# Performance work log

Hardware: AMD Instinct MI355X
Metric: run time of the kernel (lower is better)

## Reference

```python
import jax, jax.numpy as jnp
import numpy as np

N = 50000      # nodes
E = 800000     # edges
F_IN = 256
H1, D1 = 4, 32   # conv1 heads, per-head dim (hidden_features)
H2, D2 = 1, 32   # conv2 heads, per-head dim (out_features)
NEG_SLOPE = 0.2


def setup_inputs():
    key = jax.random.key(0)
    ks = jax.random.split(key, 12)
    x = jax.random.normal(ks[0], (N, F_IN), dtype=jnp.float32)
    src = jax.random.randint(ks[1], (E,), 0, N, dtype=jnp.int32)
    dst = jax.random.randint(ks[2], (E,), 0, N, dtype=jnp.int32)
    s = 0.05
    W1 = jax.random.normal(ks[3], (F_IN, H1 * D1), dtype=jnp.float32) * s
    al1 = jax.random.normal(ks[4], (H1, D1), dtype=jnp.float32) * s
    ar1 = jax.random.normal(ks[5], (H1, D1), dtype=jnp.float32) * s
    b1 = jnp.zeros((H1 * D1,), dtype=jnp.float32)
    W2 = jax.random.normal(ks[6], (H1 * D1, H2 * D2), dtype=jnp.float32) * s
    al2 = jax.random.normal(ks[7], (H2, D2), dtype=jnp.float32) * s
    ar2 = jax.random.normal(ks[8], (H2, D2), dtype=jnp.float32) * s
    b2 = jnp.zeros((H2 * D2,), dtype=jnp.float32)
    return {"x": x, "W1": W1, "al1": al1, "ar1": ar1, "b1": b1,
            "W2": W2, "al2": al2, "ar2": ar2, "b2": b2,
            "src": src, "dst": dst}


def gat_layer(x, W, al, ar, b, src, dst, H, D):
    # x: [N, F] -> feat: [N, H, D]
    feat = (x @ W).reshape(-1, H, D)
    el = jnp.sum(feat * al, axis=-1)   # [N, H]
    er = jnp.sum(feat * ar, axis=-1)   # [N, H]
    # per-edge attention logits, LeakyReLU
    e = jax.nn.leaky_relu(el[src] + er[dst], negative_slope=NEG_SLOPE)  # [E, H]
    # edge softmax over destination neighborhoods (stable)
    m = jax.ops.segment_max(e, dst, num_segments=N)          # [N, H]
    m = jnp.where(jnp.isfinite(m), m, 0.0)                   # guard zero-in-degree
    ee = jnp.exp(e - m[dst])                                 # [E, H]
    z = jax.ops.segment_sum(ee, dst, num_segments=N)         # [N, H]
    a = ee / jnp.maximum(z[dst], 1e-16)                      # [E, H]
    # weighted message aggregation
    msg = feat[src] * a[:, :, None]                          # [E, H, D]
    rst = jax.ops.segment_sum(msg, dst, num_segments=N)      # [N, H, D]
    return (rst + b.reshape(1, H, D)).reshape(-1, H * D)     # flatten(1)


def reference(x, W1, al1, ar1, b1, W2, al2, ar2, b2, src, dst):
    # dropouts are identity in eval mode; is_out_layer=True => no activation
    h = gat_layer(x, W1, al1, ar1, b1, src, dst, H1, D1)     # [N, H1*D1]
    out = gat_layer(h, W2, al2, ar2, b2, src, dst, H2, D2)   # [N, H2*D2]
    return out
```

## Files before the change

### kernel.cpp

```cpp
#include <hip/hip_runtime.h>

constexpr int F_IN = 256;
constexpr int H1 = 4, D1 = 32, F1 = H1 * D1;
constexpr int H2 = 1, D2 = 32, F2 = H2 * D2;
constexpr float NEG = 0.2f;

constexpr int BW = 128;
constexpr int NBUK_MAX = 512;
constexpr int CB = 128;

typedef short short8 __attribute__((ext_vector_type(8)));
typedef float f32x4 __attribute__((ext_vector_type(4)));

__device__ inline float bf2f(unsigned short u) {
    unsigned int x = ((unsigned int)u) << 16;
    return __builtin_bit_cast(float, x);
}
__device__ inline unsigned short f2bf(float f) {
    __bf16 h = (__bf16)f;
    return __builtin_bit_cast(unsigned short, h);
}

__global__ __launch_bounds__(256) void chist(const int* __restrict__ dst,
                                             unsigned int* __restrict__ HcT,
                                             int E, int nbuk) {
    __shared__ unsigned int h[NBUK_MAX];
    int tid = threadIdx.x;
    for (int i = tid; i < nbuk; i += 256) h[i] = 0;
    __syncthreads();
    int epb = (E + CB - 1) / CB;
    int e0 = blockIdx.x * epb, e1 = min(e0 + epb, E);
    for (int e = e0 + tid; e < e1; e += 256)
        atomicAdd(&h[dst[e] >> 7], 1u);
    __syncthreads();
    for (int i = tid; i < nbuk; i += 256) HcT[(size_t)i * CB + blockIdx.x] = h[i];
}

__global__ __launch_bounds__(512) void bscan(const unsigned int* __restrict__ HcT,
                                             unsigned int* __restrict__ Bb,
                                             unsigned int* __restrict__ S, int nbuk) {
    __shared__ unsigned int tot[NBUK_MAX];
    int t = threadIdx.x;
    unsigned int run = 0;
    if (t < nbuk) {
        const uint4* row = (const uint4*)(HcT + (size_t)t * CB);
#pragma unroll 8
        for (int b4 = 0; b4 < CB / 4; ++b4) {
            uint4 v = row[b4];
            int b = b4 * 4;
            Bb[(size_t)(b + 0) * nbuk + t] = run; run += v.x;
            Bb[(size_t)(b + 1) * nbuk + t] = run; run += v.y;
            Bb[(size_t)(b + 2) * nbuk + t] = run; run += v.z;
            Bb[(size_t)(b + 3) * nbuk + t] = run; run += v.w;
        }
    }
    tot[t] = (t < nbuk) ? run : 0;
    __syncthreads();
    for (int o = 1; o < NBUK_MAX; o <<= 1) {
        unsigned int v = (t >= o) ? tot[t - o] : 0;
        __syncthreads();
        tot[t] += v;
        __syncthreads();
    }
    if (t < nbuk) S[t] = tot[t] - run;
    if (t == nbuk - 1) S[nbuk] = tot[t];
}

__global__ __launch_bounds__(256) void cscat(const int* __restrict__ src,
                                             const int* __restrict__ dst,
                                             const unsigned int* __restrict__ Bb,
                                             const unsigned int* __restrict__ S,
                                             unsigned int* __restrict__ pairs, int E, int nbuk) {
    __shared__ unsigned int h[NBUK_MAX];
    int tid = threadIdx.x;
    for (int i = tid; i < nbuk; i += 256) h[i] = 0;
    __syncthreads();
    int epb = (E + CB - 1) / CB;
    int e0 = blockIdx.x * epb, e1 = min(e0 + epb, E);
    const unsigned int* bb = Bb + (size_t)blockIdx.x * nbuk;
    for (int e = e0 + tid; e < e1; e += 256) {
        int d = dst[e];
        int k = d >> 7;
        unsigned int r = atomicAdd(&h[k], 1u);
        unsigned int p = S[k] + bb[k] + r;
        pairs[p] = ((unsigned int)(d & 127) << 17) | (unsigned int)src[e];
    }
}

__global__ __launch_bounds__(256) void fscat(const unsigned int* __restrict__ pairs,
                                             const unsigned int* __restrict__ S,
                                             int* __restrict__ off, int* __restrict__ csr,
                                             int n, int E) {
    int k = blockIdx.x;
    int tid = threadIdx.x;
    unsigned int s0 = S[k], s1 = S[k + 1];
    __shared__ unsigned int cnt[BW];
    __shared__ unsigned int ex[BW];
    if (tid < BW) cnt[tid] = 0;
    __syncthreads();
    for (unsigned int i = s0 + tid; i < s1; i += 256)
        atomicAdd(&cnt[pairs[i] >> 17], 1u);
    __syncthreads();
    unsigned int orig = (tid < BW) ? cnt[tid] : 0;
    if (tid < BW) ex[tid] = orig;
    __syncthreads();
    for (int o = 1; o < BW; o <<= 1) {
        unsigned int v = (tid < BW && tid >= (unsigned)o) ? ex[tid - o] : 0;
        __syncthreads();
        if (tid < BW) ex[tid] += v;
        __syncthreads();
    }
    if (tid < BW) {
        ex[tid] -= orig;
        int node = k * BW + tid;
        if (node < n) off[node] = (int)(s0 + ex[tid]);
    }
    if (tid < BW) cnt[tid] = 0;
    __syncthreads();
    for (unsigned int i = s0 + tid; i < s1; i += 256) {
        unsigned int pr = pairs[i];
        int loc = pr >> 17;
        unsigned int r = atomicAdd(&cnt[loc], 1u);
        csr[s0 + ex[loc] + r] = (int)(pr & 0x1FFFFu);
    }
    if (k == 0 && tid == 0) off[n] = E;
}

__device__ inline void wsplit_one(const float* W, unsigned short* Wh, unsigned short* Wl,
                                  int idx, int C) {
    int j    = idx & 7;
    int lane = (idx >> 3) & 63;
    int t    = idx >> 9;
    int FC   = C >> 4;
    int fc   = t % FC, ks = t / FC;
    int k = ks * 32 + (lane >> 4) * 8 + j;
    int c = fc * 16 + (lane & 15);
    float v = W[(size_t)k * C + c];
    __bf16 h = (__bf16)v;
    float hv = (float)h;
    __bf16 lo = (__bf16)(v - hv);
    Wh[idx] = __builtin_bit_cast(unsigned short, h);
    Wl[idx] = __builtin_bit_cast(unsigned short, lo);
}
__global__ void wsplit_swz2(const float* __restrict__ W1, unsigned short* __restrict__ W1h,
                            unsigned short* __restrict__ W1l,
                            const float* __restrict__ W2, unsigned short* __restrict__ W2h,
                            unsigned short* __restrict__ W2l) {
    int idx = blockIdx.x * 256 + threadIdx.x;
    constexpr int N1 = F_IN * F1;
    if (idx < N1) wsplit_one(W1, W1h, W1l, idx, F1);
    else if (idx < N1 + F1 * F2) wsplit_one(W2, W2h, W2l, idx - N1, F2);
}

constexpr int BM1 = 32;
__global__ __launch_bounds__(256) void gemm1_mfma(
    const float* __restrict__ X,
    const unsigned short* __restrict__ Wh,
    const unsigned short* __restrict__ Wl,
    const float* __restrict__ alv, const float* __restrict__ arv,
    unsigned short* __restrict__ outb,
    float* __restrict__ el, float* __restrict__ er, int n)
{
    __shared__ float xs[64 * BM1 * 4];
    const int tid  = threadIdx.x;
    const int lane = tid & 63;
    const int wid  = tid >> 6;
    const int wrow = (wid >> 1) * 16;
    const int wcol = (wid & 1) * 64;
    const int wc16 = wcol >> 4;
    const int row0 = blockIdx.x * BM1;
    const int l16  = lane & 15;
    const int khi  = lane >> 4;

    {
        int r = lane & 31;
        int sub = lane >> 5;
        int gr = row0 + r;
        gr = gr < n ? gr : (n - 1);
        const float* rowp = X + (size_t)gr * F_IN;
#pragma unroll
        for (int i = 0; i < 8; ++i) {
            int kc = wid * 16 + i * 2;
            const float* srcp = rowp + (kc + sub) * 4;
            float* dstf = &xs[kc * BM1 * 4];
            __builtin_amdgcn_global_load_lds(
                (const __attribute__((address_space(1))) unsigned int*)srcp,
                (__attribute__((address_space(3))) unsigned int*)dstf,
                16, 0, 0);
        }
    }
    asm volatile("s_waitcnt vmcnt(0)" ::: "memory");
    __syncthreads();

    f32x4 acc[4];
#pragma unroll
    for (int ni = 0; ni < 4; ++ni) acc[ni] = f32x4{0.f, 0.f, 0.f, 0.f};

    const int rt = wrow + l16;

#pragma unroll
    for (int ks = 0; ks < 8; ++ks) {
        const int kc = ks * 8 + khi * 2;

        short8 bh[4], bl[4];
#pragma unroll
        for (int ni = 0; ni < 4; ++ni) {
            int base = ((ks * 8 + wc16 + ni) * 64 + lane) * 8;
            bh[ni] = *(const short8*)(Wh + base);
            bl[ni] = *(const short8*)(Wl + base);
        }

        float4 xa0 = *(const float4*)&xs[(kc + 0) * BM1 * 4 + rt * 4];
        float4 xa1 = *(const float4*)&xs[(kc + 1) * BM1 * 4 + rt * 4];
        float v[8] = {xa0.x, xa0.y, xa0.z, xa0.w, xa1.x, xa1.y, xa1.z, xa1.w};
        short8 ah, al8;
#pragma unroll
        for (int j = 0; j < 8; ++j) {
            __bf16 h = (__bf16)v[j];
            float hv = (float)h;
            __bf16 lo = (__bf16)(v[j] - hv);
            ah[j] = __builtin_bit_cast(short, h);
            al8[j] = __builtin_bit_cast(short, lo);
        }

#pragma unroll
        for (int ni = 0; ni < 4; ++ni) {
            acc[ni] = __builtin_amdgcn_mfma_f32_16x16x32_bf16(al8, bh[ni], acc[ni], 0, 0, 0);
            acc[ni] = __builtin_amdgcn_mfma_f32_16x16x32_bf16(ah, bl[ni], acc[ni], 0, 0, 0);
            acc[ni] = __builtin_amdgcn_mfma_f32_16x16x32_bf16(ah, bh[ni], acc[ni], 0, 0, 0);
        }
    }

    const int hh0 = wcol >> 5;
    float alr[2][2], arr[2][2];
#pragma unroll
    for (int t = 0; t < 2; ++t) {
        int head = hh0 + t;
        alr[t][0] = alv[head * 32 + l16];
        alr[t][1] = alv[head * 32 + 16 + l16];
        arr[t][0] = arv[head * 32 + l16];
        arr[t][1] = arv[head * 32 + 16 + l16];
    }

    int rbase = row0 + wrow + khi * 4;
#pragma unroll
    for (int rr = 0; rr < 4; ++rr) {
        int row = rbase + rr;
        bool ok = row < n;
        if (ok) {
#pragma unroll
            for (int ni = 0; ni < 4; ++ni)
                outb[(size_t)row * F1 + wcol + ni * 16 + l16] = f2bf(acc[ni][rr]);
        }
#pragma unroll
        for (int t = 0; t < 2; ++t) {
            float pel = acc[2 * t][rr] * alr[t][0] + acc[2 * t + 1][rr] * alr[t][1];
            float per = acc[2 * t][rr] * arr[t][0] + acc[2 * t + 1][rr] * arr[t][1];
#pragma unroll
            for (int o = 1; o < 16; o <<= 1) {
                pel += __shfl_xor(pel, o);
                per += __shfl_xor(per, o);
            }
            if (ok && l16 == 0) {
                el[(size_t)row * H1 + hh0 + t] = pel;
                er[(size_t)row * H1 + hh0 + t] = per;
            }
        }
    }
}

constexpr int BM2 = 64;
__global__ __launch_bounds__(256) void gemm2_mfma(
    const float* __restrict__ X,
    const unsigned short* __restrict__ Wh,
    const unsigned short* __restrict__ Wl,
    const float* __restrict__ alv, const float* __restrict__ arv,
    float* __restrict__ out,
    float* __restrict__ el, float* __restrict__ er, int n)
{
    __shared__ float xs[32 * BM2 * 4];
    const int tid  = threadIdx.x;
    const int lane = tid & 63;
    const int wid  = tid >> 6;
    const int wrow = wid * 16;
    const int row0 = blockIdx.x * BM2;
    const int l16  = lane & 15;
    const int khi  = lane >> 4;

    {
        int gr = row0 + lane;
        gr = gr < n ? gr : (n - 1);
        const float* rowp = X + (size_t)gr * F1;
#pragma unroll
        for (int i = 0; i < 8; ++i) {
            int kc = wid * 8 + i;
            const float* srcp = rowp + kc * 4;
            float* dstf = &xs[kc * BM2 * 4];
            __builtin_amdgcn_global_load_lds(
                (const __attribute__((address_space(1))) unsigned int*)srcp,
                (__attribute__((address_space(3))) unsigned int*)dstf,
                16, 0, 0);
        }
    }
    asm volatile("s_waitcnt vmcnt(0)" ::: "memory");
    __syncthreads();

    f32x4 acc[2];
#pragma unroll
    for (int ni = 0; ni < 2; ++ni) acc[ni] = f32x4{0.f, 0.f, 0.f, 0.f};

    const int rt = wrow + l16;

#pragma unroll
    for (int ks = 0; ks < 4; ++ks) {
        const int kc = ks * 8 + khi * 2;

        short8 bh[2], bl[2];
#pragma unroll
        for (int ni = 0; ni < 2; ++ni) {
            int base = ((ks * 2 + ni) * 64 + lane) * 8;
            bh[ni] = *(const short8*)(Wh + base);
            bl[ni] = *(const short8*)(Wl + base);
        }

        float4 xa0 = *(const float4*)&xs[(kc + 0) * BM2 * 4 + rt * 4];
        float4 xa1 = *(const float4*)&xs[(kc + 1) * BM2 * 4 + rt * 4];
        float v[8] = {xa0.x, xa0.y, xa0.z, xa0.w, xa1.x, xa1.y, xa1.z, xa1.w};
        short8 ah, al8;
#pragma unroll
        for (int j = 0; j < 8; ++j) {
            __bf16 h = (__bf16)v[j];
            float hv = (float)h;
            __bf16 lo = (__bf16)(v[j] - hv);
            ah[j] = __builtin_bit_cast(short, h);
            al8[j] = __builtin_bit_cast(short, lo);
        }

#pragma unroll
        for (int ni = 0; ni < 2; ++ni) {
            acc[ni] = __builtin_amdgcn_mfma_f32_16x16x32_bf16(al8, bh[ni], acc[ni], 0, 0, 0);
            acc[ni] = __builtin_amdgcn_mfma_f32_16x16x32_bf16(ah, bl[ni], acc[ni], 0, 0, 0);
            acc[ni] = __builtin_amdgcn_mfma_f32_16x16x32_bf16(ah, bh[ni], acc[ni], 0, 0, 0);
        }
    }

    float al0 = alv[l16], al1c = alv[16 + l16];
    float ar0 = arv[l16], ar1c = arv[16 + l16];

    int rbase = row0 + wrow + khi * 4;
#pragma unroll
    for (int rr = 0; rr < 4; ++rr) {
        int row = rbase + rr;
        bool ok = row < n;
        if (ok) {
#pragma unroll
            for (int ni = 0; ni < 2; ++ni)
                out[(size_t)row * F2 + ni * 16 + l16] = acc[ni][rr];
        }
        float pel = acc[0][rr] * al0 + acc[1][rr] * al1c;
        float per = acc[0][rr] * ar0 + acc[1][rr] * ar1c;
#pragma unroll
        for (int o = 1; o < 16; o <<= 1) {
            pel += __shfl_xor(pel, o);
            per += __shfl_xor(per, o);
        }
        if (ok && l16 == 0) {
            el[row] = pel;
            er[row] = per;
        }
    }
}

__global__ __launch_bounds__(256) void agg1_kernel(
    const int* __restrict__ off, const int* __restrict__ csr_src,
    const unsigned short* __restrict__ featb, const float* __restrict__ el,
    const float* __restrict__ er, const float* __restrict__ b,
    float* __restrict__ out, int n)
{
    int wid = (blockIdx.x * 256 + threadIdx.x) >> 6;
    int lane = threadIdx.x & 63;
    if (wid >= n) return;
    int c0 = (lane & 31) * 4;
    int h = (lane & 31) >> 3;
    int half = lane >> 5;
    float erv = er[(size_t)wid * H1 + h];
    float sw = 0.f;
    float4 acc = {0.f, 0.f, 0.f, 0.f};
    int jb = off[wid], je = off[wid + 1];
    int j = jb + half;
    for (; j + 6 < je; j += 8) {
        int s0 = csr_src[j];
        int s1 = csr_src[j + 2];
        int s2 = csr_src[j + 4];
        int s3 = csr_src[j + 6];
        ushort4 u0 = *(const ushort4*)(featb + (size_t)s0 * F1 + c0);
        ushort4 u1 = *(const ushort4*)(featb + (size_t)s1 * F1 + c0);
        ushort4 u2 = *(const ushort4*)(featb + (size_t)s2 * F1 + c0);
        ushort4 u3 = *(const ushort4*)(featb + (size_t)s3 * F1 + c0);
        float t0 = el[(size_t)s0 * H1 + h] + erv;
        float t1 = el[(size_t)s1 * H1 + h] + erv;
        float t2 = el[(size_t)s2 * H1 + h] + erv;
        float t3 = el[(size_t)s3 * H1 + h] + erv;
        t0 = t0 > 0.f ? t0 : NEG * t0;
        t1 = t1 > 0.f ? t1 : NEG * t1;
        t2 = t2 > 0.f ? t2 : NEG * t2;
        t3 = t3 > 0.f ? t3 : NEG * t3;
        float w0 = __expf(t0), w1 = __expf(t1), w2 = __expf(t2), w3 = __expf(t3);
        sw += (w0 + w1) + (w2 + w3);
        acc.x = fmaf(w0, bf2f(u0.x), fmaf(w1, bf2f(u1.x), fmaf(w2, bf2f(u2.x), fmaf(w3, bf2f(u3.x), acc.x))));
        acc.y = fmaf(w0, bf2f(u0.y), fmaf(w1, bf2f(u1.y), fmaf(w2, bf2f(u2.y), fmaf(w3, bf2f(u3.y), acc.y))));
        acc.z = fmaf(w0, bf2f(u0.z), fmaf(w1, bf2f(u1.z), fmaf(w2, bf2f(u2.z), fmaf(w3, bf2f(u3.z), acc.z))));
        acc.w = fmaf(w0, bf2f(u0.w), fmaf(w1, bf2f(u1.w), fmaf(w2, bf2f(u2.w), fmaf(w3, bf2f(u3.w), acc.w))));
    }
    for (; j < je; j += 2) {
        int s = csr_src[j];
        ushort4 u = *(const ushort4*)(featb + (size_t)s * F1 + c0);
        float t = el[(size_t)s * H1 + h] + erv;
        t = t > 0.f ? t : NEG * t;
        float w = __expf(t);
        sw += w;
        acc.x = fmaf(w, bf2f(u.x), acc.x);
        acc.y = fmaf(w, bf2f(u.y), acc.y);
        acc.z = fmaf(w, bf2f(u.z), acc.z);
        acc.w = fmaf(w, bf2f(u.w), acc.w);
    }
    acc.x += __shfl_xor(acc.x, 32);
    acc.y += __shfl_xor(acc.y, 32);
    acc.z += __shfl_xor(acc.z, 32);
    acc.w += __shfl_xor(acc.w, 32);
    sw    += __shfl_xor(sw, 32);
    if (half == 0) {
        float inv = 1.f / fmaxf(sw, 1e-16f);
        float4 bb = *(const float4*)(b + c0);
        float4 t = {acc.x * inv + bb.x, acc.y * inv + bb.y,
                    acc.z * inv + bb.z, acc.w * inv + bb.w};
        *(float4*)(out + (size_t)wid * F1 + c0) = t;
    }
}

__global__ __launch_bounds__(256) void agg2_kernel(
    const int* __restrict__ off, const int* __restrict__ csr_src,
    const float* __restrict__ feat, const float* __restrict__ el,
    const float* __restrict__ er, const float* __restrict__ b,
    float* __restrict__ out, int n)
{
    int wid = (blockIdx.x * 256 + threadIdx.x) >> 6;
    int lane = threadIdx.x & 63;
    if (wid >= n) return;
    int c0 = (lane & 7) * 4;
    int grp = lane >> 3;
    float erv = er[wid];
    float sw = 0.f;
    float4 acc = {0.f, 0.f, 0.f, 0.f};
    int jb = off[wid], je = off[wid + 1];
    int j = jb + grp;
    for (; j + 8 < je; j += 16) {
        int s0 = csr_src[j];
        int s1 = csr_src[j + 8];
        float4 f0 = *(const float4*)(feat + (size_t)s0 * F2 + c0);
        float4 f1 = *(const float4*)(feat + (size_t)s1 * F2 + c0);
        float t0 = el[s0] + erv;
        float t1 = el[s1] + erv;
        t0 = t0 > 0.f ? t0 : NEG * t0;
        t1 = t1 > 0.f ? t1 : NEG * t1;
        float w0 = __expf(t0);
        float w1 = __expf(t1);
        sw += w0 + w1;
        acc.x = fmaf(w0, f0.x, fmaf(w1, f1.x, acc.x));
        acc.y = fmaf(w0, f0.y, fmaf(w1, f1.y, acc.y));
        acc.z = fmaf(w0, f0.z, fmaf(w1, f1.z, acc.z));
        acc.w = fmaf(w0, f0.w, fmaf(w1, f1.w, acc.w));
    }
    for (; j < je; j += 8) {
        int s = csr_src[j];
        float4 f = *(const float4*)(feat + (size_t)s * F2 + c0);
        float t = el[s] + erv;
        t = t > 0.f ? t : NEG * t;
        float w = __expf(t);
        sw += w;
        acc.x = fmaf(w, f.x, acc.x);
        acc.y = fmaf(w, f.y, acc.y);
        acc.z = fmaf(w, f.z, acc.z);
        acc.w = fmaf(w, f.w, acc.w);
    }
#pragma unroll
    for (int o = 8; o < 64; o <<= 1) {
        acc.x += __shfl_xor(acc.x, o);
        acc.y += __shfl_xor(acc.y, o);
        acc.z += __shfl_xor(acc.z, o);
        acc.w += __shfl_xor(acc.w, o);
        sw    += __shfl_xor(sw, o);
    }
    if (lane < 8) {
        float inv = 1.f / fmaxf(sw, 1e-16f);
        float4 bb = *(const float4*)(b + c0);
        float4 t = {acc.x * inv + bb.x, acc.y * inv + bb.y,
                    acc.z * inv + bb.z, acc.w * inv + bb.w};
        *(float4*)(out + (size_t)wid * F2 + c0) = t;
    }
}

extern "C" void kernel_launch(void* const* d_in, const int* in_sizes, int n_in,
                              void* d_out, int out_size, void* d_ws, size_t ws_size,
                              hipStream_t stream) {
    const float* x   = (const float*)d_in[0];
    const float* W1  = (const float*)d_in[1];
    const float* al1 = (const float*)d_in[2];
    const float* ar1 = (const float*)d_in[3];
    const float* b1  = (const float*)d_in[4];
    const float* W2  = (const float*)d_in[5];
    const float* al2 = (const float*)d_in[6];
    const float* ar2 = (const float*)d_in[7];
    const float* b2  = (const float*)d_in[8];
    const int*   src = (const int*)d_in[9];
    const int*   dst = (const int*)d_in[10];

    const int N = in_sizes[0] / F_IN;
    const int E = in_sizes[9];
    const int NBUK = (N + BW - 1) / BW;

    char* w = (char*)d_ws;
    size_t o = 0;
    auto alloc = [&](size_t bytes) { size_t cur = o; o += (bytes + 255) & ~255ULL; return cur; };
    int*   off   = (int*)  (w + alloc((size_t)(N + 1) * 4));
    int*   csr   = (int*)  (w + alloc((size_t)E * 4));
    unsigned int* pairs = (unsigned int*)(w + alloc((size_t)E * 4));
    unsigned int* HcT = (unsigned int*)(w + alloc((size_t)CB * NBUK * 4));
    unsigned int* Bb  = (unsigned int*)(w + alloc((size_t)CB * NBUK * 4));
    unsigned int* S   = (unsigned int*)(w + alloc((size_t)(NBUK + 1) * 4));
    unsigned short* feat1b = (unsigned short*)(w + alloc((size_t)N * F1 * 2));
    float* el1   = (float*)(w + alloc((size_t)N * H1 * 4));
    float* er1   = (float*)(w + alloc((size_t)N * H1 * 4));
    float* h1    = (float*)(w + alloc((size_t)N * F1 * 4));
    float* feat2 = (float*)(w + alloc((size_t)N * F2 * 4));
    float* el2   = (float*)(w + alloc((size_t)N * H2 * 4));
    float* er2   = (float*)(w + alloc((size_t)N * H2 * 4));
    unsigned short* W1h = (unsigned short*)(w + alloc((size_t)F_IN * F1 * 2));
    unsigned short* W1l = (unsigned short*)(w + alloc((size_t)F_IN * F1 * 2));
    unsigned short* W2h = (unsigned short*)(w + alloc((size_t)F1 * F2 * 2));
    unsigned short* W2l = (unsigned short*)(w + alloc((size_t)F1 * F2 * 2));
    (void)ws_size; (void)n_in; (void)out_size;

    chist<<<CB, 256, 0, stream>>>(dst, HcT, E, NBUK);
    bscan<<<1, 512, 0, stream>>>(HcT, Bb, S, NBUK);
    cscat<<<CB, 256, 0, stream>>>(src, dst, Bb, S, pairs, E, NBUK);
    fscat<<<NBUK, 256, 0, stream>>>(pairs, S, off, csr, N, E);

    wsplit_swz2<<<(F_IN * F1 + F1 * F2 + 255) / 256, 256, 0, stream>>>(
        W1, W1h, W1l, W2, W2h, W2l);

    gemm1_mfma<<<(N + BM1 - 1) / BM1, 256, 0, stream>>>(
        x, W1h, W1l, al1, ar1, feat1b, el1, er1, N);
    agg1_kernel<<<(N + 3) / 4, 256, 0, stream>>>(off, csr, feat1b, el1, er1, b1, h1, N);

    gemm2_mfma<<<(N + BM2 - 1) / BM2, 256, 0, stream>>>(
        h1, W2h, W2l, al2, ar2, feat2, el2, er2, N);
    agg2_kernel<<<(N + 3) / 4, 256, 0, stream>>>(off, csr, feat2, el2, er2, b2, (float*)d_out, N);
}
```

Measured before the change: 149.7 us.

## Double gemm1 row tile and prefetch weight fragments one k-step ahead

Gemm1 now handles 64 rows per block, with each wave computing two 16-row MFMA tiles, so every loaded weight fragment (high and low bf16 halves) is reused across twice as many rows. The weight loads for the next k-step are double-buffered in registers so global loads overlap the current MFMAs. This halves the grid size and increases register and LDS use per block, which may reduce occupancy.

```diff
diff --git a/kernel.cpp b/kernel.cpp
--- a/kernel.cpp
+++ b/kernel.cpp
@@ -152,7 +152,7 @@
     else if (idx < N1 + F1 * F2) wsplit_one(W2, W2h, W2l, idx - N1, F2);
 }
 
-constexpr int BM1 = 32;
+constexpr int BM1 = 64;
 __global__ __launch_bounds__(256) void gemm1_mfma(
     const float* __restrict__ X,
     const unsigned short* __restrict__ Wh,
@@ -165,7 +165,7 @@
     const int tid  = threadIdx.x;
     const int lane = tid & 63;
     const int wid  = tid >> 6;
-    const int wrow = (wid >> 1) * 16;
+    const int wrow = (wid >> 1) * 32;
     const int wcol = (wid & 1) * 64;
     const int wc16 = wcol >> 4;
     const int row0 = blockIdx.x * BM1;
@@ -173,15 +173,13 @@
     const int khi  = lane >> 4;
 
     {
-        int r = lane & 31;
-        int sub = lane >> 5;
-        int gr = row0 + r;
+        int gr = row0 + lane;
         gr = gr < n ? gr : (n - 1);
         const float* rowp = X + (size_t)gr * F_IN;
 #pragma unroll
-        for (int i = 0; i < 8; ++i) {
-            int kc = wid * 16 + i * 2;
-            const float* srcp = rowp + (kc + sub) * 4;
+        for (int i = 0; i < 16; ++i) {
+            int kc = wid * 16 + i;
+            const float* srcp = rowp + kc * 4;
             float* dstf = &xs[kc * BM1 * 4];
             __builtin_amdgcn_global_load_lds(
                 (const __attribute__((address_space(1))) unsigned int*)srcp,
@@ -192,43 +190,58 @@
     asm volatile("s_waitcnt vmcnt(0)" ::: "memory");
     __syncthreads();
 
-    f32x4 acc[4];
-#pragma unroll
-    for (int ni = 0; ni < 4; ++ni) acc[ni] = f32x4{0.f, 0.f, 0.f, 0.f};
-
-    const int rt = wrow + l16;
+    f32x4 acc[2][4];
+#pragma unroll
+    for (int mi = 0; mi < 2; ++mi)
+#pragma unroll
+        for (int ni = 0; ni < 4; ++ni) acc[mi][ni] = f32x4{0.f, 0.f, 0.f, 0.f};
+
+    short8 bh[2][4], bl[2][4];
+#pragma unroll
+    for (int ni = 0; ni < 4; ++ni) {
+        int base = ((0 * 8 + wc16 + ni) * 64 + lane) * 8;
+        bh[0][ni] = *(const short8*)(Wh + base);
+        bl[0][ni] = *(const short8*)(Wl + base);
+    }
 
 #pragma unroll
     for (int ks = 0; ks < 8; ++ks) {
+        const int cur = ks & 1, nxt = cur ^ 1;
+        if (ks < 7) {
+#pragma unroll
+            for (int ni = 0; ni < 4; ++ni) {
+                int base = (((ks + 1) * 8 + wc16 + ni) * 64 + lane) * 8;
+                bh[nxt][ni] = *(const short8*)(Wh + base);
+                bl[nxt][ni] = *(const short8*)(Wl + base);
+            }
+        }
+
         const int kc = ks * 8 + khi * 2;
-
-        short8 bh[4], bl[4];
-#pragma unroll
-        for (int ni = 0; ni < 4; ++ni) {
-            int base = ((ks * 8 + wc16 + ni) * 64 + lane) * 8;
-            bh[ni] = *(const short8*)(Wh + base);
-            bl[ni] = *(const short8*)(Wl + base);
-        }
-
-        float4 xa0 = *(const float4*)&xs[(kc + 0) * BM1 * 4 + rt * 4];
-        float4 xa1 = *(const float4*)&xs[(kc + 1) * BM1 * 4 + rt * 4];
-        float v[8] = {xa0.x, xa0.y, xa0.z, xa0.w, xa1.x, xa1.y, xa1.z, xa1.w};
-        short8 ah, al8;
-#pragma unroll
-        for (int j = 0; j < 8; ++j) {
-            __bf16 h = (__bf16)v[j];
-            float hv = (float)h;
-            __bf16 lo = (__bf16)(v[j] - hv);
-            ah[j] = __builtin_bit_cast(short, h);
-            al8[j] = __builtin_bit_cast(short, lo);
-        }
-
-#pragma unroll
-        for (int ni = 0; ni < 4; ++ni) {
-            acc[ni] = __builtin_amdgcn_mfma_f32_16x16x32_bf16(al8, bh[ni], acc[ni], 0, 0, 0);
-            acc[ni] = __builtin_amdgcn_mfma_f32_16x16x32_bf16(ah, bl[ni], acc[ni], 0, 0, 0);
-            acc[ni] = __builtin_amdgcn_mfma_f32_16x16x32_bf16(ah, bh[ni], acc[ni], 0, 0, 0);
-        }
+        short8 ah[2], al8[2];
+#pragma unroll
+        for (int mi = 0; mi < 2; ++mi) {
+            const int rt = wrow + mi * 16 + l16;
+            float4 xa0 = *(const float4*)&xs[(kc + 0) * BM1 * 4 + rt * 4];
+            float4 xa1 = *(const float4*)&xs[(kc + 1) * BM1 * 4 + rt * 4];
+            float v[8] = {xa0.x, xa0.y, xa0.z, xa0.w, xa1.x, xa1.y, xa1.z, xa1.w};
+#pragma unroll
+            for (int j = 0; j < 8; ++j) {
+                __bf16 h = (__bf16)v[j];
+                float hv = (float)h;
+                __bf16 lo = (__bf16)(v[j] - hv);
+                ah[mi][j] = __builtin_bit_cast(short, h);
+                al8[mi][j] = __builtin_bit_cast(short, lo);
+            }
+        }
+
+#pragma unroll
+        for (int mi = 0; mi < 2; ++mi)
+#pragma unroll
+            for (int ni = 0; ni < 4; ++ni) {
+                acc[mi][ni] = __builtin_amdgcn_mfma_f32_16x16x32_bf16(al8[mi], bh[cur][ni], acc[mi][ni], 0, 0, 0);
+                acc[mi][ni] = __builtin_amdgcn_mfma_f32_16x16x32_bf16(ah[mi], bl[cur][ni], acc[mi][ni], 0, 0, 0);
+                acc[mi][ni] = __builtin_amdgcn_mfma_f32_16x16x32_bf16(ah[mi], bh[cur][ni], acc[mi][ni], 0, 0, 0);
+            }
     }
 
     const int hh0 = wcol >> 5;
@@ -242,28 +255,31 @@
         arr[t][1] = arv[head * 32 + 16 + l16];
     }
 
-    int rbase = row0 + wrow + khi * 4;
-#pragma unroll
-    for (int rr = 0; rr < 4; ++rr) {
-        int row = rbase + rr;
-        bool ok = row < n;
-        if (ok) {
-#pragma unroll
-            for (int ni = 0; ni < 4; ++ni)
-                outb[(size_t)row * F1 + wcol + ni * 16 + l16] = f2bf(acc[ni][rr]);
-        }
-#pragma unroll
-        for (int t = 0; t < 2; ++t) {
-            float pel = acc[2 * t][rr] * alr[t][0] + acc[2 * t + 1][rr] * alr[t][1];
-            float per = acc[2 * t][rr] * arr[t][0] + acc[2 * t + 1][rr] * arr[t][1];
-#pragma unroll
-            for (int o = 1; o < 16; o <<= 1) {
-                pel += __shfl_xor(pel, o);
-                per += __shfl_xor(per, o);
+#pragma unroll
+    for (int mi = 0; mi < 2; ++mi) {
+        int rbase = row0 + wrow + mi * 16 + khi * 4;
+#pragma unroll
+        for (int rr = 0; rr < 4; ++rr) {
+            int row = rbase + rr;
+            bool ok = row < n;
+            if (ok) {
+#pragma unroll
+                for (int ni = 0; ni < 4; ++ni)
+                    outb[(size_t)row * F1 + wcol + ni * 16 + l16] = f2bf(acc[mi][ni][rr]);
             }
-            if (ok && l16 == 0) {
-                el[(size_t)row * H1 + hh0 + t] = pel;
-                er[(size_t)row * H1 + hh0 + t] = per;
+#pragma unroll
+            for (int t = 0; t < 2; ++t) {
+                float pel = acc[mi][2 * t][rr] * alr[t][0] + acc[mi][2 * t + 1][rr] * alr[t][1];
+                float per = acc[mi][2 * t][rr] * arr[t][0] + acc[mi][2 * t + 1][rr] * arr[t][1];
+#pragma unroll
+                for (int o = 1; o < 16; o <<= 1) {
+                    pel += __shfl_xor(pel, o);
+                    per += __shfl_xor(per, o);
+                }
+                if (ok && l16 == 0) {
+                    el[(size_t)row * H1 + hh0 + t] = pel;
+                    er[(size_t)row * H1 + hh0 + t] = per;
+                }
             }
         }
     }
```

Result: no change. 150.4 us (+0.5%).
